# Kernel tuning notes

Measured on AMD Instinct MI355X. Metric: run time of the kernel, lower is better.

Reference implementation:

```python
import jax, jax.numpy as jnp
import numpy as np

N = 100000      # nodes
E = 1600000     # edges (avg degree 16)
F_IN = 128
H1, H2, C = 200, 50, 10


def _lin(key, fin, fout):
    # Glorot-uniform-ish init
    lim = (6.0 / (fin + fout)) ** 0.5
    return jax.random.uniform(key, (fin, fout), jnp.float32, -lim, lim)


def setup_inputs() -> dict:
    key = jax.random.key(0)
    ks = jax.random.split(key, 11)
    x = jax.random.normal(ks[0], (N, F_IN), jnp.float32)
    edge_index = jax.random.randint(ks[1], (2, E), 0, N, jnp.int32)
    return {
        "x": x,
        "edge_index": edge_index,
        "W_l1": _lin(ks[2], F_IN, H1), "b1": jnp.zeros((H1,), jnp.float32), "W_r1": _lin(ks[3], F_IN, H1),
        "W_l2": _lin(ks[4], H1, H2),   "b2": jnp.zeros((H2,), jnp.float32), "W_r2": _lin(ks[5], H1, H2),
        "W_l3": _lin(ks[6], H2, C),    "b3": jnp.zeros((C,), jnp.float32),  "W_r3": _lin(ks[7], H2, C),
    }


def _sage_conv_max(x, src, dst, W_l, b, W_r):
    # gather neighbor (source) features, scatter-max into destination nodes
    agg = jax.ops.segment_max(x[src], dst, num_segments=N)   # [N, F]
    agg = jnp.where(jnp.isfinite(agg), agg, 0.0)             # empty segments -> 0 (PyG behavior)
    return agg @ W_l + b + x @ W_r


def reference(x, edge_index, W_l1, b1, W_r1, W_l2, b2, W_r2, W_l3, b3, W_r3):
    src, dst = edge_index[0], edge_index[1]
    h = _sage_conv_max(x, src, dst, W_l1, b1, W_r1)   # [N, 200]
    h = _sage_conv_max(h, src, dst, W_l2, b2, W_r2)   # [N, 50]
    h = _sage_conv_max(h, src, dst, W_l3, b3, W_r3)   # [N, 10]
    return jax.nn.log_softmax(h, axis=1)
```

## Files before the change

kernel.cpp:

```cpp
#include <hip/hip_runtime.h>
#include <cstdint>
#include <cstddef>

#define N_NODES 100000
#define N_EDGES 1600000
#define F_IN    128
#define H1D     200
#define H2D     50
#define NCLS    10

#define P1 256
#define P2 416
#define P3 128
#define H2OFF 56
#define X1PD 48
#define X2PD 80

#define BSH 9
#define BMASK 511
#define NB 196
#define EPB 8192

typedef __attribute__((ext_vector_type(8))) short short8;
typedef __attribute__((ext_vector_type(4))) float f32x4;

__device__ __forceinline__ unsigned short f2b(float f) {
    union { float f; uint32_t u; } v; v.f = f;
    uint32_t u = v.u;
    return (unsigned short)((u + 0x7fffu + ((u >> 16) & 1u)) >> 16);
}
__device__ __forceinline__ float b2f(unsigned short b) {
    union { uint32_t u; float f; } v; v.u = ((uint32_t)b) << 16;
    return v.f;
}
__device__ __forceinline__ void upk(uint32_t p, float& a, float& b) {
    union { uint32_t u; float f; } lo, hi;
    lo.u = (p & 0xffffu) << 16;
    hi.u = p & 0xffff0000u;
    a = lo.f; b = hi.f;
}

__device__ __forceinline__ uint32_t b2s12(unsigned short h) {
    int e = (int)(h & 0x7FFF) - 15488;
    e = e < 0 ? 0 : (e > 2047 ? 2047 : e);
    return (h & 0x8000) ? (uint32_t)(2047 - e) : (uint32_t)(2048 + e);
}
__device__ __forceinline__ unsigned short s122b(uint32_t t) {
    if (t >= 2048u) { uint32_t mag = t - 2048u; return mag ? (unsigned short)(mag + 15488u) : (unsigned short)0; }
    uint32_t mag = 2047u - t;   return mag ? (unsigned short)(0x8000u | (mag + 15488u)) : (unsigned short)0;
}
__device__ __forceinline__ void pack12(const uint32_t* t, uint32_t& d0, uint32_t& d1, uint32_t& d2) {
    d0 = t[0] | (t[1] << 12) | (t[2] << 24);
    d1 = (t[2] >> 8) | (t[3] << 4) | (t[4] << 16) | (t[5] << 28);
    d2 = (t[5] >> 4) | (t[6] << 8) | (t[7] << 20);
}

__device__ __forceinline__ int block_excl_scan_256(int v, int* wsum) {
    const int tid = threadIdx.x;
    const int lane = tid & 63;
    const int wid = tid >> 6;
    int incl = v;
    #pragma unroll
    for (int off = 1; off < 64; off <<= 1) {
        int t = __shfl_up(incl, off, 64);
        if (lane >= off) incl += t;
    }
    if (lane == 63) wsum[wid] = incl;
    __syncthreads();
    if (tid == 0) {
        int s = 0;
        #pragma unroll
        for (int k = 0; k < 4; k++) { int t = wsum[k]; wsum[k] = s; s += t; }
    }
    __syncthreads();
    return wsum[wid] + incl - v;
}

__global__ __launch_bounds__(256) void csr_p0(const int* __restrict__ dst,
                                              int* __restrict__ bcnt, int E) {
    __shared__ int c[256];
    const int tid = threadIdx.x;
    c[tid] = 0;
    __syncthreads();
    const int base = blockIdx.x * EPB;
    #pragma unroll 4
    for (int i = 0; i < EPB / 256; i++) {
        int e = base + i * 256 + tid;
        if (e < E) atomicAdd(&c[dst[e] >> BSH], 1);
    }
    __syncthreads();
    int v = c[tid];
    if (v > 0) atomicAdd(&bcnt[tid], v);
}

__global__ __launch_bounds__(256) void csr_bscan(const int* __restrict__ bcnt,
                                                 int* __restrict__ g_bbase,
                                                 int* __restrict__ g_bcur) {
    __shared__ int wsum[4];
    const int tid = threadIdx.x;
    int v = (tid < NB) ? bcnt[tid] : 0;
    int excl = block_excl_scan_256(v, wsum);
    if (tid < NB) { g_bbase[tid] = excl; g_bcur[tid] = excl; }
    if (tid == NB) g_bbase[NB] = excl;
}

__global__ __launch_bounds__(256) void csr_p1(const int* __restrict__ src,
                                              const int* __restrict__ dst,
                                              int* __restrict__ g_bcur,
                                              uint32_t* __restrict__ staging, int E) {
    __shared__ int cnt[256];
    __shared__ int base_s[256];
    const int tid = threadIdx.x;
    const int base = blockIdx.x * EPB;
    cnt[tid] = 0;
    __syncthreads();
    #pragma unroll 4
    for (int i = 0; i < EPB / 256; i++) {
        int e = base + i * 256 + tid;
        if (e < E) atomicAdd(&cnt[dst[e] >> BSH], 1);
    }
    __syncthreads();
    int v = cnt[tid];
    if (v > 0) base_s[tid] = atomicAdd(&g_bcur[tid], v);
    cnt[tid] = 0;
    __syncthreads();
    #pragma unroll 4
    for (int i = 0; i < EPB / 256; i++) {
        int e = base + i * 256 + tid;
        if (e < E) {
            int d = dst[e], s = src[e];
            int b = d >> BSH;
            int r = atomicAdd(&cnt[b], 1);
            staging[base_s[b] + r] = ((uint32_t)s << BSH) | (uint32_t)(d & BMASK);
        }
    }
}

__global__ __launch_bounds__(256) void csr_p2(const uint32_t* __restrict__ staging,
                                              const int* __restrict__ g_bbase,
                                              int* __restrict__ row_ptr,
                                              int* __restrict__ col_src, int N, int E) {
    __shared__ int cnt[512];
    __shared__ int wsum[4];
    const int tid = threadIdx.x;
    const int nodeBase = blockIdx.x << BSH;
    cnt[tid] = 0; cnt[tid + 256] = 0;
    __syncthreads();
    const int lo = g_bbase[blockIdx.x];
    const int hi = g_bbase[blockIdx.x + 1];
    for (int j = lo + tid; j < hi; j += 256)
        atomicAdd(&cnt[staging[j] & BMASK], 1);
    __syncthreads();
    int v0 = cnt[2 * tid], v1 = cnt[2 * tid + 1];
    int pexcl = block_excl_scan_256(v0 + v1, wsum);
    __syncthreads();
    cnt[2 * tid]     = lo + pexcl;
    cnt[2 * tid + 1] = lo + pexcl + v0;
    int node0 = nodeBase + 2 * tid;
    if (node0 < N)     row_ptr[node0]     = lo + pexcl;
    if (node0 + 1 < N) row_ptr[node0 + 1] = lo + pexcl + v0;
    __syncthreads();
    for (int j = lo + tid; j < hi; j += 256) {
        uint32_t rec = staging[j];
        int p = atomicAdd(&cnt[rec & BMASK], 1);
        col_src[p] = (int)(rec >> BSH);
    }
    if (blockIdx.x == 0 && tid == 0) row_ptr[N] = E;
}

__global__ void build_bt_all(const float* __restrict__ Wl1, const float* __restrict__ Wr1,
                             const float* __restrict__ Wl2, const float* __restrict__ Wr2,
                             const float* __restrict__ Wl3, const float* __restrict__ Wr3,
                             unsigned short* __restrict__ Bt1,
                             unsigned short* __restrict__ Bt2,
                             unsigned short* __restrict__ Bt3) {
    constexpr int S1 = H1D * P1, S2 = H2D * P2, S3 = NCLS * P3;
    int idx = blockIdx.x * blockDim.x + threadIdx.x;
    if (idx < S1) {
        int m = idx / P1, k = idx - m * P1;
        float v = 0.0f;
        if (k < F_IN)            v = Wl1[(size_t)k * H1D + m];
        else if (k < 2 * F_IN)   v = Wr1[(size_t)(k - F_IN) * H1D + m];
        Bt1[idx] = f2b(v);
    } else if (idx < S1 + S2) {
        int j = idx - S1;
        int m = j / P2, k = j - m * P2;
        float v = 0.0f;
        if (k < H1D)             v = Wl2[(size_t)k * H2D + m];
        else if (k < 2 * H1D)    v = Wr2[(size_t)(k - H1D) * H2D + m];
        Bt2[j] = f2b(v);
    } else if (idx < S1 + S2 + S3) {
        int j = idx - S1 - S2;
        int m = j / P3, k = j - m * P3;
        float v = 0.0f;
        if (k < H2D)                          v = Wl3[(size_t)k * NCLS + m];
        else if (k >= H2OFF && k < H2OFF+H2D) v = Wr3[(size_t)(k - H2OFF) * NCLS + m];
        Bt3[j] = f2b(v);
    }
}

__global__ void conv_x_kernel(const float* __restrict__ x,
                              unsigned short* __restrict__ A1,
                              uint32_t* __restrict__ X12, int N) {
    int idx = blockIdx.x * blockDim.x + threadIdx.x;
    if (idx >= N * 16) return;
    int row = idx >> 4, g = idx & 15;
    const float* xp = x + (size_t)row * F_IN + g * 8;
    unsigned short h[8];
    #pragma unroll
    for (int i = 0; i < 8; i++) h[i] = f2b(xp[i]);
    ushort4 o0 = {h[0], h[1], h[2], h[3]};
    ushort4 o1 = {h[4], h[5], h[6], h[7]};
    *(ushort4*)(A1 + (size_t)row * P1 + F_IN + g * 8) = o0;
    *(ushort4*)(A1 + (size_t)row * P1 + F_IN + g * 8 + 4) = o1;
    uint32_t t[8];
    #pragma unroll
    for (int i = 0; i < 8; i++) t[i] = b2s12(h[i]);
    uint32_t d0, d1, d2;
    pack12(t, d0, d1, d2);
    uint32_t* op = X12 + (size_t)row * X1PD + g * 3;
    op[0] = d0; op[1] = d1; op[2] = d2;
}

__global__ void pad_a3_kernel(unsigned short* __restrict__ A3, int N) {
    int idx = blockIdx.x * blockDim.x + threadIdx.x;
    if (idx >= N * 28) return;
    int r = idx / 28, c = idx - r * 28;
    int col = (c < 6) ? (50 + c) : (100 + c);
    A3[(size_t)r * P3 + col] = 0;
}

template <int F, int G, int PITCHD>
__global__ __launch_bounds__(256) void agg_max_12(
    const uint32_t* __restrict__ X12,
    const int* __restrict__ row_ptr, const int* __restrict__ col_src,
    unsigned short* __restrict__ O, int opitch, int N) {
    static_assert(G == 16 || G == 32, "G must be 16/32");
    const int wave = (blockIdx.x * blockDim.x + threadIdx.x) >> 6;
    const int lane = threadIdx.x & 63;
    if (wave >= N) return;
    const int beg = row_ptr[wave];
    const int end = row_ptr[wave + 1];
    constexpr int LOG2G = (G == 16) ? 4 : 5;
    constexpr int EPW = 64 / G;
    const int l = lane & (G - 1);
    const int grp = lane >> LOG2G;
    const int f0 = l * 8;
    const bool act = (f0 < F);

    uint32_t t[8];
    #pragma unroll
    for (int i = 0; i < 8; i++) t[i] = 0u;

    auto mrg = [&](uint32_t d0, uint32_t d1, uint32_t d2) {
        uint32_t v;
        v = d0 & 0xFFFu;                        t[0] = t[0] > v ? t[0] : v;
        v = (d0 >> 12) & 0xFFFu;                t[1] = t[1] > v ? t[1] : v;
        v = (d0 >> 24) | ((d1 & 0xFu) << 8);    t[2] = t[2] > v ? t[2] : v;
        v = (d1 >> 4) & 0xFFFu;                 t[3] = t[3] > v ? t[3] : v;
        v = (d1 >> 16) & 0xFFFu;                t[4] = t[4] > v ? t[4] : v;
        v = (d1 >> 28) | ((d2 & 0xFFu) << 4);   t[5] = t[5] > v ? t[5] : v;
        v = (d2 >> 8) & 0xFFFu;                 t[6] = t[6] > v ? t[6] : v;
        v = d2 >> 20;                           t[7] = t[7] > v ? t[7] : v;
    };

    int j = beg + grp;
    for (; j + EPW < end; j += 2 * EPW) {
        int s0 = col_src[j];
        int s1 = col_src[j + EPW];
        uint32_t a0 = 0, a1 = 0, a2 = 0, b0 = 0, b1 = 0, b2 = 0;
        if (act) {
            const uint32_t* p0 = X12 + (size_t)s0 * PITCHD + l * 3;
            const uint32_t* p1 = X12 + (size_t)s1 * PITCHD + l * 3;
            a0 = p0[0]; a1 = p0[1]; a2 = p0[2];
            b0 = p1[0]; b1 = p1[1]; b2 = p1[2];
        }
        mrg(a0, a1, a2);
        mrg(b0, b1, b2);
    }
    if (j < end && act) {
        const uint32_t* p = X12 + (size_t)col_src[j] * PITCHD + l * 3;
        mrg(p[0], p[1], p[2]);
    }

    #pragma unroll
    for (int off = G; off < 64; off <<= 1) {
        #pragma unroll
        for (int i = 0; i < 8; i++) {
            uint32_t v = (uint32_t)__shfl_xor((int)t[i], off, 64);
            t[i] = t[i] > v ? t[i] : v;
        }
    }

    if (grp == 0 && act) {
        unsigned short* op = O + (size_t)wave * opitch;
        uint4 o = {0u, 0u, 0u, 0u};
        if (beg != end) {
            unsigned short h[8];
            #pragma unroll
            for (int i = 0; i < 8; i++) h[i] = s122b(t[i]);
            o.x = (uint32_t)h[0] | ((uint32_t)h[1] << 16);
            o.y = (uint32_t)h[2] | ((uint32_t)h[3] << 16);
            o.z = (uint32_t)h[4] | ((uint32_t)h[5] << 16);
            o.w = (uint32_t)h[6] | ((uint32_t)h[7] << 16);
        }
        *(uint4*)(op + f0) = o;
    }
}

template <int F, int G>
__global__ __launch_bounds__(256) void agg_max_v3(
    const unsigned short* __restrict__ X, int xpitch,
    const int* __restrict__ row_ptr, const int* __restrict__ col_src,
    unsigned short* __restrict__ O, int opitch, int N) {
    static_assert(G == 8 || G == 16 || G == 32, "G must be 8/16/32");
    static_assert(G * 8 >= F, "group must cover F");
    const int wave = (blockIdx.x * blockDim.x + threadIdx.x) >> 6;
    const int lane = threadIdx.x & 63;
    if (wave >= N) return;
    const int beg = row_ptr[wave];
    const int end = row_ptr[wave + 1];
    constexpr int LOG2G = (G == 8) ? 3 : ((G == 16) ? 4 : 5);
    constexpr int EPW = 64 / G;
    const int l = lane & (G - 1);
    const int grp = lane >> LOG2G;
    const int f0 = l * 8;
    const bool act = (f0 < F);

    float m[8];
    #pragma unroll
    for (int i = 0; i < 8; i++) m[i] = -INFINITY;

    auto ld = [&](int s) -> uint4 {
        if (act) return *(const uint4*)(X + (size_t)s * xpitch + f0);
        return (uint4){0u, 0u, 0u, 0u};
    };
    auto mrg = [&](const uint4& v) {
        if (act) {
            float a, b;
            upk(v.x, a, b); m[0] = fmaxf(m[0], a); m[1] = fmaxf(m[1], b);
            upk(v.y, a, b); m[2] = fmaxf(m[2], a); m[3] = fmaxf(m[3], b);
            upk(v.z, a, b); m[4] = fmaxf(m[4], a); m[5] = fmaxf(m[5], b);
            upk(v.w, a, b); m[6] = fmaxf(m[6], a); m[7] = fmaxf(m[7], b);
        }
    };

    int j = beg + grp;
    for (; j + EPW < end; j += 2 * EPW) {
        int s0 = col_src[j];
        int s1 = col_src[j + EPW];
        uint4 v0 = ld(s0), v1 = ld(s1);
        mrg(v0); mrg(v1);
    }
    if (j < end) mrg(ld(col_src[j]));

    #pragma unroll
    for (int off = G; off < 64; off <<= 1) {
        #pragma unroll
        for (int i = 0; i < 8; i++)
            m[i] = fmaxf(m[i], __shfl_xor(m[i], off, 64));
    }

    if (grp == 0 && act) {
        unsigned short* op = O + (size_t)wave * opitch;
        const bool empty = (beg == end);
        if (f0 + 8 <= F) {
            uint4 o = {0u, 0u, 0u, 0u};
            if (!empty) {
                o.x = (uint32_t)f2b(m[0]) | ((uint32_t)f2b(m[1]) << 16);
                o.y = (uint32_t)f2b(m[2]) | ((uint32_t)f2b(m[3]) << 16);
                o.z = (uint32_t)f2b(m[4]) | ((uint32_t)f2b(m[5]) << 16);
                o.w = (uint32_t)f2b(m[6]) | ((uint32_t)f2b(m[7]) << 16);
            }
            *(uint4*)(op + f0) = o;
        } else {
            for (int i = 0; f0 + i < F; i++)
                op[f0 + i] = empty ? (unsigned short)0 : f2b(m[i]);
        }
    }
}

template <int NCT, int MODE>
__global__ __launch_bounds__(256) void gemm_mfma_v3(
    const unsigned short* __restrict__ A, int P,
    const unsigned short* __restrict__ Bt,
    const float* __restrict__ bias,
    float* __restrict__ Cf,
    unsigned short* __restrict__ Cb, int cbPitch, int cbOff,
    uint32_t* __restrict__ X12out,
    unsigned short* __restrict__ Htab,
    int Nrows, int M) {
    constexpr int ABSZ = 2560 + NCT * 640;
    constexpr int SSZ = (MODE == 1) ? (ABSZ > 12800 ? ABSZ : 12800) : ABSZ;
    __shared__ short smem[SSZ];
    short* As = smem;
    short* Bs = smem + 2560;
    short* Hs = smem;
    const int tid = threadIdx.x;
    const int wv = tid >> 6;
    const int lane = tid & 63;
    const int q = lane >> 4;
    const int mi = lane & 15;
    const int rowBase = blockIdx.x * 64;

    f32x4 acc[NCT];
    #pragma unroll
    for (int c = 0; c < NCT; c++) acc[c] = (f32x4){0.f, 0.f, 0.f, 0.f};

    const int srow = tid >> 2;
    const int sseg = tid & 3;
    const int grow = rowBase + srow;
    constexpr int BSLOTS = NCT * 64;
    constexpr int BITERS = (BSLOTS + 255) / 256;

    for (int kt = 0; kt < P; kt += 32) {
        uint4 va = {0u, 0u, 0u, 0u};
        if (grow < Nrows) va = *(const uint4*)(A + (size_t)grow * P + kt + sseg * 8);
        *(uint4*)(&As[srow * 40 + sseg * 8]) = va;
        #pragma unroll
        for (int i = 0; i < BITERS; i++) {
            int slot = i * 256 + tid;
            if (slot < BSLOTS) {
                int br = slot >> 2;
                int bs = slot & 3;
                uint4 vb = {0u, 0u, 0u, 0u};
                if (br < M) vb = *(const uint4*)(Bt + (size_t)br * P + kt + bs * 8);
                *(uint4*)(&Bs[br * 40 + bs * 8]) = vb;
            }
        }
        __syncthreads();
        short8 a = *(const short8*)(&As[(wv * 16 + mi) * 40 + q * 8]);
        #pragma unroll
        for (int c = 0; c < NCT; c++) {
            short8 b = *(const short8*)(&Bs[(c * 16 + mi) * 40 + q * 8]);
            acc[c] = __builtin_amdgcn_mfma_f32_16x16x32_bf16(a, b, acc[c], 0, 0, 0);
        }
        __syncthreads();
    }

    if constexpr (MODE == 3) {
        float bv = (mi < M) ? bias[mi] : 0.0f;
        #pragma unroll
        for (int r = 0; r < 4; r++) {
            float v = acc[0][r] + bv;
            float mx = (mi < M) ? v : -INFINITY;
            #pragma unroll
            for (int off = 1; off < 16; off <<= 1)
                mx = fmaxf(mx, __shfl_xor(mx, off, 64));
            float ex = (mi < M) ? expf(v - mx) : 0.0f;
            float sm = ex;
            #pragma unroll
            for (int off = 1; off < 16; off <<= 1)
                sm += __shfl_xor(sm, off, 64);
            int row = rowBase + wv * 16 + q * 4 + r;
            if (mi < M && row < Nrows)
                Cf[(size_t)row * M + mi] = v - mx - logf(sm);
        }
    } else {
        #pragma unroll
        for (int c = 0; c < NCT; c++) {
            int col = c * 16 + mi;
            if (col >= M) continue;
            float bv = bias[col];
            #pragma unroll
            for (int r = 0; r < 4; r++) {
                int row = rowBase + wv * 16 + q * 4 + r;
                if (row >= Nrows) continue;
                float v = acc[c][r] + bv;
                unsigned short h = f2b(v);
                Cb[(size_t)row * cbPitch + cbOff + col] = h;
                if constexpr (MODE == 1)
                    Hs[(wv * 16 + q * 4 + r) * 200 + col] = (short)h;
                if constexpr (MODE == 2)
                    if (col < H2D) Htab[(size_t)row * 64 + col] = h;
            }
        }
        if constexpr (MODE == 1) {
            for (int k = tid; k < 64 * 16; k += 256) {
                int r = k >> 4, c = k & 15;
                int row = rowBase + r;
                if (row < Nrows) Cb[(size_t)row * cbPitch + 2 * H1D + c] = 0;
            }
            __syncthreads();
            for (int k = tid; k < 64 * 25; k += 256) {
                int r = k / 25, g = k - r * 25;
                int row = rowBase + r;
                if (row >= Nrows) continue;
                const short* hp = &Hs[r * 200 + g * 8];
                uint32_t t[8];
                #pragma unroll
                for (int i = 0; i < 8; i++) t[i] = b2s12((unsigned short)hp[i]);
                uint32_t d0, d1, d2;
                pack12(t, d0, d1, d2);
                uint32_t* op = X12out + (size_t)row * X2PD + g * 3;
                op[0] = d0; op[1] = d1; op[2] = d2;
            }
        }
    }
}

extern "C" void kernel_launch(void* const* d_in, const int* in_sizes, int n_in,
                              void* d_out, int out_size, void* d_ws, size_t ws_size,
                              hipStream_t stream) {
    const float* x    = (const float*)d_in[0];
    const int*   eidx = (const int*)d_in[1];
    const float* Wl1  = (const float*)d_in[2];
    const float* b1   = (const float*)d_in[3];
    const float* Wr1  = (const float*)d_in[4];
    const float* Wl2  = (const float*)d_in[5];
    const float* b2   = (const float*)d_in[6];
    const float* Wr2  = (const float*)d_in[7];
    const float* Wl3  = (const float*)d_in[8];
    const float* b3   = (const float*)d_in[9];
    const float* Wr3  = (const float*)d_in[10];
    const int* srcp = eidx;
    const int* dstp = eidx + N_EDGES;
    float* out = (float*)d_out;
    (void)ws_size; (void)in_sizes; (void)n_in; (void)out_size;

    char* w = (char*)d_ws;
    size_t off = 0;
    auto alloc = [&](size_t bytes) -> char* {
        char* p = w + off;
        off += (bytes + 255) & ~(size_t)255;
        return p;
    };
    int* bcnt     = (int*)alloc(sizeof(int) * 256);
    int* g_bbase  = (int*)alloc(sizeof(int) * 256);
    int* g_bcur   = (int*)alloc(sizeof(int) * 256);
    int* row_ptr  = (int*)alloc(sizeof(int) * (N_NODES + 1));
    int* col_src  = (int*)alloc(sizeof(int) * N_EDGES);
    char* Z = alloc(32u * 1024 * 1024);
    uint32_t* staging = (uint32_t*)Z;
    uint32_t* X12_1   = (uint32_t*)(Z + 8u * 1024 * 1024);
    uint32_t* X12_2   = (uint32_t*)Z;
    unsigned short* A1  = (unsigned short*)alloc(sizeof(short) * (size_t)N_NODES * P1);
    unsigned short* A2  = (unsigned short*)alloc(sizeof(short) * (size_t)N_NODES * P2);
    unsigned short* A3  = (unsigned short*)alloc(sizeof(short) * (size_t)N_NODES * P3);
    unsigned short* Bt1 = (unsigned short*)alloc(sizeof(short) * H1D * P1);
    unsigned short* Bt2 = (unsigned short*)alloc(sizeof(short) * H2D * P2);
    unsigned short* Bt3 = (unsigned short*)alloc(sizeof(short) * NCLS * P3);
    unsigned short* X16_3 = A1;

    const int EDGE_BLKS = (N_EDGES + EPB - 1) / EPB;
    hipMemsetAsync(bcnt, 0, sizeof(int) * 256, stream);
    csr_p0<<<EDGE_BLKS, 256, 0, stream>>>(dstp, bcnt, N_EDGES);
    csr_bscan<<<1, 256, 0, stream>>>(bcnt, g_bbase, g_bcur);
    csr_p1<<<EDGE_BLKS, 256, 0, stream>>>(srcp, dstp, g_bcur, staging, N_EDGES);
    csr_p2<<<NB, 256, 0, stream>>>(staging, g_bbase, row_ptr, col_src, N_NODES, N_EDGES);

    constexpr int BT_TOTAL = H1D * P1 + H2D * P2 + NCLS * P3;
    build_bt_all<<<(BT_TOTAL + 255) / 256, 256, 0, stream>>>(Wl1, Wr1, Wl2, Wr2, Wl3, Wr3, Bt1, Bt2, Bt3);
    conv_x_kernel<<<(N_NODES * 16 + 255) / 256, 256, 0, stream>>>(x, A1, X12_1, N_NODES);
    pad_a3_kernel<<<(N_NODES * 28 + 255) / 256, 256, 0, stream>>>(A3, N_NODES);

    const int aggBlocks = (N_NODES + 3) / 4;
    const int rowTiles = (N_NODES + 63) / 64;

    agg_max_12<F_IN, 16, X1PD><<<aggBlocks, 256, 0, stream>>>(X12_1, row_ptr, col_src, A1, P1, N_NODES);
    gemm_mfma_v3<13, 1><<<rowTiles, 256, 0, stream>>>(A1, P1, Bt1, b1, nullptr, A2, P2, H1D, X12_2, nullptr, N_NODES, H1D);

    agg_max_12<H1D, 32, X2PD><<<aggBlocks, 256, 0, stream>>>(X12_2, row_ptr, col_src, A2, P2, N_NODES);
    gemm_mfma_v3<4, 2><<<rowTiles, 256, 0, stream>>>(A2, P2, Bt2, b2, nullptr, A3, P3, H2OFF, nullptr, X16_3, N_NODES, H2D);

    agg_max_v3<H2D, 8><<<aggBlocks, 256, 0, stream>>>(X16_3, 64, row_ptr, col_src, A3, P3, N_NODES);
    gemm_mfma_v3<1, 3><<<rowTiles, 256, 0, stream>>>(A3, P3, Bt3, b3, out, nullptr, 0, 0, nullptr, nullptr, N_NODES, NCLS);
}
```

Baseline: 487.9 us.

## Fuse layer-3 aggregation with GEMM and softmax; drop CSR count pass via fixed-capacity buckets

The CSR build no longer runs a separate count pass and scan before scattering. Each destination bucket gets a fixed staging capacity (CAP), and the scan runs afterward on the final cursors. Layer 3's max aggregation, its 10-class MFMA GEMM and the log-softmax are fused into one kernel that builds the A tile in LDS, so the A3 buffer, the padding kernel and its global round trip go away. Layer 2's GEMM now writes only the Htab table and zeroes its pad columns. The risks are bucket overflow if any bucket exceeds CAP edges, and lower parallelism in the fused aggregation, where each wave loops serially over 16 nodes.

```diff
diff --git a/kernel.cpp b/kernel.cpp
--- a/kernel.cpp
+++ b/kernel.cpp
@@ -20,6 +20,7 @@
 #define BMASK 511
 #define NB 196
 #define EPB 8192
+#define CAP 9216
 
 typedef __attribute__((ext_vector_type(8))) short short8;
 typedef __attribute__((ext_vector_type(4))) float f32x4;
@@ -76,32 +77,9 @@
     return wsum[wid] + incl - v;
 }
 
-__global__ __launch_bounds__(256) void csr_p0(const int* __restrict__ dst,
-                                              int* __restrict__ bcnt, int E) {
-    __shared__ int c[256];
-    const int tid = threadIdx.x;
-    c[tid] = 0;
-    __syncthreads();
-    const int base = blockIdx.x * EPB;
-    #pragma unroll 4
-    for (int i = 0; i < EPB / 256; i++) {
-        int e = base + i * 256 + tid;
-        if (e < E) atomicAdd(&c[dst[e] >> BSH], 1);
-    }
-    __syncthreads();
-    int v = c[tid];
-    if (v > 0) atomicAdd(&bcnt[tid], v);
-}
-
-__global__ __launch_bounds__(256) void csr_bscan(const int* __restrict__ bcnt,
-                                                 int* __restrict__ g_bbase,
-                                                 int* __restrict__ g_bcur) {
-    __shared__ int wsum[4];
-    const int tid = threadIdx.x;
-    int v = (tid < NB) ? bcnt[tid] : 0;
-    int excl = block_excl_scan_256(v, wsum);
-    if (tid < NB) { g_bbase[tid] = excl; g_bcur[tid] = excl; }
-    if (tid == NB) g_bbase[NB] = excl;
+__global__ void csr_init(int* __restrict__ g_bcur) {
+    int t = threadIdx.x;
+    if (t < NB) g_bcur[t] = t * CAP;
 }
 
 __global__ __launch_bounds__(256) void csr_p1(const int* __restrict__ src,
@@ -136,7 +114,17 @@
     }
 }
 
+__global__ __launch_bounds__(256) void csr_bscan(const int* __restrict__ g_bcur,
+                                                 int* __restrict__ g_bbase) {
+    __shared__ int wsum[4];
+    const int tid = threadIdx.x;
+    int v = (tid < NB) ? (g_bcur[tid] - tid * CAP) : 0;
+    int excl = block_excl_scan_256(v, wsum);
+    if (tid <= NB) g_bbase[tid] = excl;
+}
+
 __global__ __launch_bounds__(256) void csr_p2(const uint32_t* __restrict__ staging,
+                                              const int* __restrict__ g_bcur,
                                               const int* __restrict__ g_bbase,
                                               int* __restrict__ row_ptr,
                                               int* __restrict__ col_src, int N, int E) {
@@ -146,21 +134,22 @@
     const int nodeBase = blockIdx.x << BSH;
     cnt[tid] = 0; cnt[tid + 256] = 0;
     __syncthreads();
-    const int lo = g_bbase[blockIdx.x];
-    const int hi = g_bbase[blockIdx.x + 1];
-    for (int j = lo + tid; j < hi; j += 256)
+    const int lo_s = blockIdx.x * CAP;
+    const int hi_s = g_bcur[blockIdx.x];
+    const int colBase = g_bbase[blockIdx.x];
+    for (int j = lo_s + tid; j < hi_s; j += 256)
         atomicAdd(&cnt[staging[j] & BMASK], 1);
     __syncthreads();
     int v0 = cnt[2 * tid], v1 = cnt[2 * tid + 1];
     int pexcl = block_excl_scan_256(v0 + v1, wsum);
     __syncthreads();
-    cnt[2 * tid]     = lo + pexcl;
-    cnt[2 * tid + 1] = lo + pexcl + v0;
+    cnt[2 * tid]     = colBase + pexcl;
+    cnt[2 * tid + 1] = colBase + pexcl + v0;
     int node0 = nodeBase + 2 * tid;
-    if (node0 < N)     row_ptr[node0]     = lo + pexcl;
-    if (node0 + 1 < N) row_ptr[node0 + 1] = lo + pexcl + v0;
-    __syncthreads();
-    for (int j = lo + tid; j < hi; j += 256) {
+    if (node0 < N)     row_ptr[node0]     = colBase + pexcl;
+    if (node0 + 1 < N) row_ptr[node0 + 1] = colBase + pexcl + v0;
+    __syncthreads();
+    for (int j = lo_s + tid; j < hi_s; j += 256) {
         uint32_t rec = staging[j];
         int p = atomicAdd(&cnt[rec & BMASK], 1);
         col_src[p] = (int)(rec >> BSH);
@@ -222,14 +211,6 @@
     op[0] = d0; op[1] = d1; op[2] = d2;
 }
 
-__global__ void pad_a3_kernel(unsigned short* __restrict__ A3, int N) {
-    int idx = blockIdx.x * blockDim.x + threadIdx.x;
-    if (idx >= N * 28) return;
-    int r = idx / 28, c = idx - r * 28;
-    int col = (c < 6) ? (50 + c) : (100 + c);
-    A3[(size_t)r * P3 + col] = 0;
-}
-
 template <int F, int G, int PITCHD>
 __global__ __launch_bounds__(256) void agg_max_12(
     const uint32_t* __restrict__ X12,
@@ -308,84 +289,11 @@
     }
 }
 
-template <int F, int G>
-__global__ __launch_bounds__(256) void agg_max_v3(
-    const unsigned short* __restrict__ X, int xpitch,
-    const int* __restrict__ row_ptr, const int* __restrict__ col_src,
-    unsigned short* __restrict__ O, int opitch, int N) {
-    static_assert(G == 8 || G == 16 || G == 32, "G must be 8/16/32");
-    static_assert(G * 8 >= F, "group must cover F");
-    const int wave = (blockIdx.x * blockDim.x + threadIdx.x) >> 6;
-    const int lane = threadIdx.x & 63;
-    if (wave >= N) return;
-    const int beg = row_ptr[wave];
-    const int end = row_ptr[wave + 1];
-    constexpr int LOG2G = (G == 8) ? 3 : ((G == 16) ? 4 : 5);
-    constexpr int EPW = 64 / G;
-    const int l = lane & (G - 1);
-    const int grp = lane >> LOG2G;
-    const int f0 = l * 8;
-    const bool act = (f0 < F);
-
-    float m[8];
-    #pragma unroll
-    for (int i = 0; i < 8; i++) m[i] = -INFINITY;
-
-    auto ld = [&](int s) -> uint4 {
-        if (act) return *(const uint4*)(X + (size_t)s * xpitch + f0);
-        return (uint4){0u, 0u, 0u, 0u};
-    };
-    auto mrg = [&](const uint4& v) {
-        if (act) {
-            float a, b;
-            upk(v.x, a, b); m[0] = fmaxf(m[0], a); m[1] = fmaxf(m[1], b);
-            upk(v.y, a, b); m[2] = fmaxf(m[2], a); m[3] = fmaxf(m[3], b);
-            upk(v.z, a, b); m[4] = fmaxf(m[4], a); m[5] = fmaxf(m[5], b);
-            upk(v.w, a, b); m[6] = fmaxf(m[6], a); m[7] = fmaxf(m[7], b);
-        }
-    };
-
-    int j = beg + grp;
-    for (; j + EPW < end; j += 2 * EPW) {
-        int s0 = col_src[j];
-        int s1 = col_src[j + EPW];
-        uint4 v0 = ld(s0), v1 = ld(s1);
-        mrg(v0); mrg(v1);
-    }
-    if (j < end) mrg(ld(col_src[j]));
-
-    #pragma unroll
-    for (int off = G; off < 64; off <<= 1) {
-        #pragma unroll
-        for (int i = 0; i < 8; i++)
-            m[i] = fmaxf(m[i], __shfl_xor(m[i], off, 64));
-    }
-
-    if (grp == 0 && act) {
-        unsigned short* op = O + (size_t)wave * opitch;
-        const bool empty = (beg == end);
-        if (f0 + 8 <= F) {
-            uint4 o = {0u, 0u, 0u, 0u};
-            if (!empty) {
-                o.x = (uint32_t)f2b(m[0]) | ((uint32_t)f2b(m[1]) << 16);
-                o.y = (uint32_t)f2b(m[2]) | ((uint32_t)f2b(m[3]) << 16);
-                o.z = (uint32_t)f2b(m[4]) | ((uint32_t)f2b(m[5]) << 16);
-                o.w = (uint32_t)f2b(m[6]) | ((uint32_t)f2b(m[7]) << 16);
-            }
-            *(uint4*)(op + f0) = o;
-        } else {
-            for (int i = 0; f0 + i < F; i++)
-                op[f0 + i] = empty ? (unsigned short)0 : f2b(m[i]);
-        }
-    }
-}
-
 template <int NCT, int MODE>
 __global__ __launch_bounds__(256) void gemm_mfma_v3(
     const unsigned short* __restrict__ A, int P,
     const unsigned short* __restrict__ Bt,
     const float* __restrict__ bias,
-    float* __restrict__ Cf,
     unsigned short* __restrict__ Cb, int cbPitch, int cbOff,
     uint32_t* __restrict__ X12out,
     unsigned short* __restrict__ Htab,
@@ -438,64 +346,176 @@
         __syncthreads();
     }
 
-    if constexpr (MODE == 3) {
-        float bv = (mi < M) ? bias[mi] : 0.0f;
+    #pragma unroll
+    for (int c = 0; c < NCT; c++) {
+        int col = c * 16 + mi;
+        if (col >= M) continue;
+        float bv = bias[col];
         #pragma unroll
         for (int r = 0; r < 4; r++) {
-            float v = acc[0][r] + bv;
-            float mx = (mi < M) ? v : -INFINITY;
+            int row = rowBase + wv * 16 + q * 4 + r;
+            if (row >= Nrows) continue;
+            float v = acc[c][r] + bv;
+            unsigned short h = f2b(v);
+            if constexpr (MODE == 1) {
+                Cb[(size_t)row * cbPitch + cbOff + col] = h;
+                Hs[(wv * 16 + q * 4 + r) * 200 + col] = (short)h;
+            }
+            if constexpr (MODE == 2) {
+                if (col < H2D) Htab[(size_t)row * 64 + col] = h;
+            }
+        }
+    }
+    if constexpr (MODE == 1) {
+        for (int k = tid; k < 64 * 16; k += 256) {
+            int r = k >> 4, c = k & 15;
+            int row = rowBase + r;
+            if (row < Nrows) Cb[(size_t)row * cbPitch + 2 * H1D + c] = 0;
+        }
+        __syncthreads();
+        for (int k = tid; k < 64 * 25; k += 256) {
+            int r = k / 25, g = k - r * 25;
+            int row = rowBase + r;
+            if (row >= Nrows) continue;
+            const short* hp = &Hs[r * 200 + g * 8];
+            uint32_t t[8];
             #pragma unroll
-            for (int off = 1; off < 16; off <<= 1)
-                mx = fmaxf(mx, __shfl_xor(mx, off, 64));
-            float ex = (mi < M) ? expf(v - mx) : 0.0f;
-            float sm = ex;
+            for (int i = 0; i < 8; i++) t[i] = b2s12((unsigned short)hp[i]);
+            uint32_t d0, d1, d2;
+            pack12(t, d0, d1, d2);
+            uint32_t* op = X12out + (size_t)row * X2PD + g * 3;
+            op[0] = d0; op[1] = d1; op[2] = d2;
+        }
+    }
+    if constexpr (MODE == 2) {
+        for (int k = tid; k < 64 * 14; k += 256) {
+            int r = k / 14, c = k - r * 14;
+            int row = rowBase + r;
+            if (row < Nrows) Htab[(size_t)row * 64 + H2D + c] = 0;
+        }
+    }
+}
+
+__global__ __launch_bounds__(256) void layer3_fused(
+    const unsigned short* __restrict__ Htab,
+    const int* __restrict__ row_ptr, const int* __restrict__ col_src,
+    const unsigned short* __restrict__ Bt,
+    const float* __restrict__ bias,
+    float* __restrict__ out, int N) {
+    __shared__ short As[64 * 136];
+    __shared__ short Bs[640];
+    const int tid = threadIdx.x;
+    const int wv = tid >> 6;
+    const int lane = tid & 63;
+    const int rowBase = blockIdx.x * 64;
+
+    {
+        const int l = lane & 7;
+        const int grp = lane >> 3;
+        const int f0 = l * 8;
+        const bool act = (f0 < H2D);
+        for (int n = 0; n < 16; n++) {
+            int node = rowBase + wv * 16 + n;
+            int beg = 0, end = 0;
+            if (node < N) { beg = row_ptr[node]; end = row_ptr[node + 1]; }
+            float m[8];
             #pragma unroll
-            for (int off = 1; off < 16; off <<= 1)
-                sm += __shfl_xor(sm, off, 64);
-            int row = rowBase + wv * 16 + q * 4 + r;
-            if (mi < M && row < Nrows)
-                Cf[(size_t)row * M + mi] = v - mx - logf(sm);
-        }
-    } else {
-        #pragma unroll
-        for (int c = 0; c < NCT; c++) {
-            int col = c * 16 + mi;
-            if (col >= M) continue;
-            float bv = bias[col];
+            for (int i = 0; i < 8; i++) m[i] = -INFINITY;
+            auto ld = [&](int s) -> uint4 {
+                if (act) return *(const uint4*)(Htab + (size_t)s * 64 + f0);
+                return (uint4){0u, 0u, 0u, 0u};
+            };
+            auto mrg = [&](const uint4& v) {
+                if (act) {
+                    float a, b;
+                    upk(v.x, a, b); m[0] = fmaxf(m[0], a); m[1] = fmaxf(m[1], b);
+                    upk(v.y, a, b); m[2] = fmaxf(m[2], a); m[3] = fmaxf(m[3], b);
+                    upk(v.z, a, b); m[4] = fmaxf(m[4], a); m[5] = fmaxf(m[5], b);
+                    upk(v.w, a, b); m[6] = fmaxf(m[6], a); m[7] = fmaxf(m[7], b);
+                }
+            };
+            int j = beg + grp;
+            for (; j + 8 < end; j += 16) {
+                int s0 = col_src[j];
+                int s1 = col_src[j + 8];
+                uint4 v0 = ld(s0), v1 = ld(s1);
+                mrg(v0); mrg(v1);
+            }
+            if (j < end) mrg(ld(col_src[j]));
             #pragma unroll
-            for (int r = 0; r < 4; r++) {
-                int row = rowBase + wv * 16 + q * 4 + r;
-                if (row >= Nrows) continue;
-                float v = acc[c][r] + bv;
-                unsigned short h = f2b(v);
-                Cb[(size_t)row * cbPitch + cbOff + col] = h;
-                if constexpr (MODE == 1)
-                    Hs[(wv * 16 + q * 4 + r) * 200 + col] = (short)h;
-                if constexpr (MODE == 2)
-                    if (col < H2D) Htab[(size_t)row * 64 + col] = h;
+            for (int off = 8; off < 64; off <<= 1) {
+                #pragma unroll
+                for (int i = 0; i < 8; i++)
+                    m[i] = fmaxf(m[i], __shfl_xor(m[i], off, 64));
             }
-        }
-        if constexpr (MODE == 1) {
-            for (int k = tid; k < 64 * 16; k += 256) {
-                int r = k >> 4, c = k & 15;
-                int row = rowBase + r;
-                if (row < Nrows) Cb[(size_t)row * cbPitch + 2 * H1D + c] = 0;
+            if (grp == 0 && act) {
+                short* op = &As[(wv * 16 + n) * 136];
+                const bool empty = (beg == end);
+                if (f0 + 8 <= H2D) {
+                    uint4 o = {0u, 0u, 0u, 0u};
+                    if (!empty) {
+                        o.x = (uint32_t)f2b(m[0]) | ((uint32_t)f2b(m[1]) << 16);
+                        o.y = (uint32_t)f2b(m[2]) | ((uint32_t)f2b(m[3]) << 16);
+                        o.z = (uint32_t)f2b(m[4]) | ((uint32_t)f2b(m[5]) << 16);
+                        o.w = (uint32_t)f2b(m[6]) | ((uint32_t)f2b(m[7]) << 16);
+                    }
+                    *(uint4*)(op + f0) = o;
+                } else {
+                    uint32_t o2 = empty ? 0u
+                        : ((uint32_t)f2b(m[0]) | ((uint32_t)f2b(m[1]) << 16));
+                    *(uint32_t*)(op + f0) = o2;
+                }
             }
-            __syncthreads();
-            for (int k = tid; k < 64 * 25; k += 256) {
-                int r = k / 25, g = k - r * 25;
-                int row = rowBase + r;
-                if (row >= Nrows) continue;
-                const short* hp = &Hs[r * 200 + g * 8];
-                uint32_t t[8];
-                #pragma unroll
-                for (int i = 0; i < 8; i++) t[i] = b2s12((unsigned short)hp[i]);
-                uint32_t d0, d1, d2;
-                pack12(t, d0, d1, d2);
-                uint32_t* op = X12out + (size_t)row * X2PD + g * 3;
-                op[0] = d0; op[1] = d1; op[2] = d2;
-            }
-        }
+        }
+    }
+    for (int k = tid; k < 64 * 25; k += 256) {
+        int r = k / 25, c = (k - r * 25) * 2;
+        int node = rowBase + r;
+        uint32_t v = 0;
+        if (node < N) v = *(const uint32_t*)(Htab + (size_t)node * 64 + c);
+        *(uint32_t*)(&As[r * 136 + H2OFF + c]) = v;
+    }
+    for (int k = tid; k < 64 * 28; k += 256) {
+        int r = k / 28, c = k - r * 28;
+        int col = (c < 6) ? (50 + c) : (100 + c);
+        As[r * 136 + col] = 0;
+    }
+    __syncthreads();
+
+    const int q = lane >> 4;
+    const int mi = lane & 15;
+    f32x4 acc = (f32x4){0.f, 0.f, 0.f, 0.f};
+    for (int kt = 0; kt < P3; kt += 32) {
+        if (tid < 64) {
+            int br = tid >> 2;
+            int bs = tid & 3;
+            uint4 vb = {0u, 0u, 0u, 0u};
+            if (br < NCLS) vb = *(const uint4*)(Bt + (size_t)br * P3 + kt + bs * 8);
+            *(uint4*)(&Bs[br * 40 + bs * 8]) = vb;
+        }
+        __syncthreads();
+        short8 a = *(const short8*)(&As[(wv * 16 + mi) * 136 + kt + q * 8]);
+        short8 b = *(const short8*)(&Bs[mi * 40 + q * 8]);
+        acc = __builtin_amdgcn_mfma_f32_16x16x32_bf16(a, b, acc, 0, 0, 0);
+        __syncthreads();
+    }
+
+    float bv = (mi < NCLS) ? bias[mi] : 0.0f;
+    #pragma unroll
+    for (int r = 0; r < 4; r++) {
+        float v = acc[r] + bv;
+        float mx = (mi < NCLS) ? v : -INFINITY;
+        #pragma unroll
+        for (int off = 1; off < 16; off <<= 1)
+            mx = fmaxf(mx, __shfl_xor(mx, off, 64));
+        float ex = (mi < NCLS) ? expf(v - mx) : 0.0f;
+        float sm = ex;
+        #pragma unroll
+        for (int off = 1; off < 16; off <<= 1)
+            sm += __shfl_xor(sm, off, 64);
+        int row = rowBase + wv * 16 + q * 4 + r;
+        if (mi < NCLS && row < N)
+            out[(size_t)row * NCLS + mi] = v - mx - logf(sm);
     }
 }
 
@@ -525,7 +545,6 @@
         off += (bytes + 255) & ~(size_t)255;
         return p;
     };
-    int* bcnt     = (int*)alloc(sizeof(int) * 256);
     int* g_bbase  = (int*)alloc(sizeof(int) * 256);
     int* g_bcur   = (int*)alloc(sizeof(int) * 256);
     int* row_ptr  = (int*)alloc(sizeof(int) * (N_NODES + 1));
@@ -536,33 +555,29 @@
     uint32_t* X12_2   = (uint32_t*)Z;
     unsigned short* A1  = (unsigned short*)alloc(sizeof(short) * (size_t)N_NODES * P1);
     unsigned short* A2  = (unsigned short*)alloc(sizeof(short) * (size_t)N_NODES * P2);
-    unsigned short* A3  = (unsigned short*)alloc(sizeof(short) * (size_t)N_NODES * P3);
     unsigned short* Bt1 = (unsigned short*)alloc(sizeof(short) * H1D * P1);
     unsigned short* Bt2 = (unsigned short*)alloc(sizeof(short) * H2D * P2);
     unsigned short* Bt3 = (unsigned short*)alloc(sizeof(short) * NCLS * P3);
     unsigned short* X16_3 = A1;
 
     const int EDGE_BLKS = (N_EDGES + EPB - 1) / EPB;
-    hipMemsetAsync(bcnt, 0, sizeof(int) * 256, stream);
-    csr_p0<<<EDGE_BLKS, 256, 0, stream>>>(dstp, bcnt, N_EDGES);
-    csr_bscan<<<1, 256, 0, stream>>>(bcnt, g_bbase, g_bcur);
+    csr_init<<<1, 256, 0, stream>>>(g_bcur);
     csr_p1<<<EDGE_BLKS, 256, 0, stream>>>(srcp, dstp, g_bcur, staging, N_EDGES);
-    csr_p2<<<NB, 256, 0, stream>>>(staging, g_bbase, row_ptr, col_src, N_NODES, N_EDGES);
+    csr_bscan<<<1, 256, 0, stream>>>(g_bcur, g_bbase);
+    csr_p2<<<NB, 256, 0, stream>>>(staging, g_bcur, g_bbase, row_ptr, col_src, N_NODES, N_EDGES);
 
     constexpr int BT_TOTAL = H1D * P1 + H2D * P2 + NCLS * P3;
     build_bt_all<<<(BT_TOTAL + 255) / 256, 256, 0, stream>>>(Wl1, Wr1, Wl2, Wr2, Wl3, Wr3, Bt1, Bt2, Bt3);
     conv_x_kernel<<<(N_NODES * 16 + 255) / 256, 256, 0, stream>>>(x, A1, X12_1, N_NODES);
-    pad_a3_kernel<<<(N_NODES * 28 + 255) / 256, 256, 0, stream>>>(A3, N_NODES);
 
     const int aggBlocks = (N_NODES + 3) / 4;
     const int rowTiles = (N_NODES + 63) / 64;
 
     agg_max_12<F_IN, 16, X1PD><<<aggBlocks, 256, 0, stream>>>(X12_1, row_ptr, col_src, A1, P1, N_NODES);
-    gemm_mfma_v3<13, 1><<<rowTiles, 256, 0, stream>>>(A1, P1, Bt1, b1, nullptr, A2, P2, H1D, X12_2, nullptr, N_NODES, H1D);
+    gemm_mfma_v3<13, 1><<<rowTiles, 256, 0, stream>>>(A1, P1, Bt1, b1, A2, P2, H1D, X12_2, nullptr, N_NODES, H1D);
 
     agg_max_12<H1D, 32, X2PD><<<aggBlocks, 256, 0, stream>>>(X12_2, row_ptr, col_src, A2, P2, N_NODES);
-    gemm_mfma_v3<4, 2><<<rowTiles, 256, 0, stream>>>(A2, P2, Bt2, b2, nullptr, A3, P3, H2OFF, nullptr, X16_3, N_NODES, H2D);
-
-    agg_max_v3<H2D, 8><<<aggBlocks, 256, 0, stream>>>(X16_3, 64, row_ptr, col_src, A3, P3, N_NODES);
-    gemm_mfma_v3<1, 3><<<rowTiles, 256, 0, stream>>>(A3, P3, Bt3, b3, out, nullptr, 0, 0, nullptr, nullptr, N_NODES, NCLS);
-}
+    gemm_mfma_v3<4, 2><<<rowTiles, 256, 0, stream>>>(A2, P2, Bt2, b2, nullptr, 0, 0, nullptr, X16_3, N_NODES, H2D);
+
+    layer3_fused<<<rowTiles, 256, 0, stream>>>(X16_3, row_ptr, col_src, Bt3, b3, out, N_NODES);
+}
```

After: 464.4 us. 4.8% less time.
